# Kernel tuning notes

Measured on AMD Instinct MI355X. Metric: run time of the kernel, lower is better.

Reference implementation:

```python
import jax, jax.numpy as jnp
import numpy as np

H = W = 512
P = H * W          # total superpixel member pixels
N_SP = 1024        # number of superpixels


def _conv(x, w, b):
    # x: [N,C,H,W], w: [O,I,3,3] -> [N,O,H,W], SAME padding
    y = jax.lax.conv_general_dilated(
        x, w, window_strides=(1, 1), padding='SAME',
        dimension_numbers=('NCHW', 'OIHW', 'NCHW'))
    return y + b[None, :, None, None]


def _embed(raw, w1, b1, w2, b2, w3, b3):
    h = jax.nn.relu(_conv(raw, w1, b1))
    h = jax.nn.relu(_conv(h, w2, b2))
    return _conv(h, w3, b3)  # [1, 10, H, W]


def setup_inputs() -> dict:
    key = jax.random.key(0)
    ks = jax.random.split(key, 6)
    raw = jax.random.normal(ks[0], (1, 1, H, W), dtype=jnp.float32)
    w1 = jax.random.normal(ks[1], (64, 1, 3, 3), dtype=jnp.float32) * 0.3
    b1 = jnp.zeros((64,), jnp.float32)
    w2 = jax.random.normal(ks[2], (64, 64, 3, 3), dtype=jnp.float32) * 0.05
    b2 = jnp.zeros((64,), jnp.float32)
    w3 = jax.random.normal(ks[3], (10, 64, 3, 3), dtype=jnp.float32) * 0.05
    b3 = jnp.zeros((10,), jnp.float32)
    pix_rc = jax.random.randint(ks[4], (P, 2), 0, H, dtype=jnp.int32)
    seg_ids = jax.random.randint(ks[5], (P,), 0, N_SP, dtype=jnp.int32)
    return {"raw": raw, "w1": w1, "b1": b1, "w2": w2, "b2": b2,
            "w3": w3, "b3": b3, "pix_rc": pix_rc, "seg_ids": seg_ids,
            "n_sp": N_SP}


def reference(raw, w1, b1, w2, b2, w3, b3, pix_rc, seg_ids, n_sp):
    feats = _embed(raw, w1, b1, w2, b2, w3, b3)  # [1, C, H, W]
    f = feats[0]                                  # [C, H, W]
    # gather per-pixel feature vectors: [P, C]
    vals = f[:, pix_rc[:, 0], pix_rc[:, 1]].T
    # scatter-mean over superpixels (= per-sp sum / mass)
    sums = jax.ops.segment_sum(vals, seg_ids, num_segments=n_sp)      # [n_sp, C]
    cnts = jax.ops.segment_sum(jnp.ones((vals.shape[0],), vals.dtype),
                               seg_ids, num_segments=n_sp)            # [n_sp]
    return sums / jnp.maximum(cnts, 1.0)[:, None]
```

## Files before the change

kernel.cpp:

```cpp
#include <hip/hip_runtime.h>

typedef __attribute__((ext_vector_type(8))) short short8;
typedef __attribute__((ext_vector_type(4))) float f32x4;

constexpr int H = 512, W = 512;
constexpr int P = H * W;
constexpr int NSP = 1024;
constexpr int SBLK = 512;
constexpr int FGRP = 16;

__device__ inline unsigned short f2bf(float f) {
  unsigned u = __builtin_bit_cast(unsigned, f);
  unsigned r = (u + 0x7fffu + ((u >> 16) & 1u)) >> 16;
  return (unsigned short)r;
}
__device__ inline float bflo(unsigned u) { return __builtin_bit_cast(float, u << 16); }
__device__ inline float bfhi(unsigned u) { return __builtin_bit_cast(float, u & 0xffff0000u); }

__device__ inline int xcd_swz(int b, int cpx) { return (b & 7) * cpx + (b >> 3); }

__global__ __launch_bounds__(256) void prep_k(const float* __restrict__ w2,
                                              const float* __restrict__ w3,
                                              unsigned short* __restrict__ wt2s,
                                              unsigned short* __restrict__ wt3s) {
  int i = blockIdx.x * 256 + threadIdx.x;
  if (i < 36864) {
    int k = i >> 11;
    int t = (i >> 3) & 255;
    int e = i & 7;
    int r = t >> 2, sp = t & 3, s = sp ^ ((r >> 2) & 3);
    int tap = k >> 1, ic = (k & 1) * 32 + s * 8 + e;
    wt2s[i] = f2bf(w2[r * 576 + ic * 9 + tap]);
  } else if (i < 46080) {
    int j = i - 36864;
    int k = j >> 9;
    int t = (j >> 3) & 63;
    int e = j & 7;
    int r = t >> 2, sp = t & 3, s = sp ^ ((r >> 2) & 3);
    int tap = k >> 1, ic = (k & 1) * 32 + s * 8 + e;
    wt3s[j] = (r < 10) ? f2bf(w3[r * 576 + ic * 9 + tap]) : (unsigned short)0;
  }
}

__global__ __launch_bounds__(512, 4) void conv123_k(const float* __restrict__ raw,
                                                    const float* __restrict__ w1,
                                                    const float* __restrict__ b1,
                                                    const unsigned short* __restrict__ wts2,
                                                    const float* __restrict__ b2,
                                                    const unsigned short* __restrict__ wts3,
                                                    const float* __restrict__ b3,
                                                    unsigned short* __restrict__ feats) {
  constexpr int WCS = 2048;
  __shared__ __align__(16) unsigned short acts[448 * 64];
  __shared__ __align__(16) unsigned short wbuf[9216];
  __shared__ unsigned short rawtb[14 * 38 + 12];
  int tid = threadIdx.x;
  int lane = tid & 63, wave = tid >> 6;
  int logical = xcd_swz(blockIdx.x, 128);
  int tilex = logical & 15, tiley = logical >> 4;
  int c0 = tilex * 32, r0 = tiley * 8;

  if (tid < 256) {
#pragma unroll
    for (int k0 = 0; k0 < 3; ++k0) {
      const unsigned short* src = wts2 + (size_t)k0 * WCS + tid * 8;
      unsigned short* dstb = wbuf + (k0 & 3) * WCS + wave * 512;
      __builtin_amdgcn_global_load_lds((const __attribute__((address_space(1))) void*)src,
                                       (__attribute__((address_space(3))) void*)dstb, 16, 0, 0);
    }
  }
  for (int i = tid; i < 532; i += 512) {
    int rr = i / 38, cc = i - rr * 38;
    int gr = r0 + rr - 3, gc = c0 + cc - 3;
    bool ok = ((unsigned)gr < 512u) && ((unsigned)gc < 512u);
    rawtb[i] = ok ? f2bf(raw[gr * 512 + gc]) : (unsigned short)0;
  }

  int q = lane >> 4, n = lane & 15;
  int og1 = wave & 3;
  short8 a1f;
  {
    short av[8];
#pragma unroll
    for (int e = 0; e < 8; ++e) av[e] = 0;
    int oc = og1 * 16 + n;
    if (q == 0) {
#pragma unroll
      for (int e = 0; e < 8; ++e) av[e] = (short)f2bf(w1[oc * 9 + e]);
    } else if (q == 1) {
      av[0] = (short)f2bf(w1[oc * 9 + 8]);
    }
    a1f = (short8){av[0], av[1], av[2], av[3], av[4], av[5], av[6], av[7]};
  }
  float bb1[4];
#pragma unroll
  for (int r2 = 0; r2 < 4; ++r2) bb1[r2] = b1[og1 * 16 + q * 4 + r2];
  __syncthreads();

  char* actw = (char*)acts;
  int hhalf = wave >> 2;
  for (int i1 = 0; i1 < 14; ++i1) {
    int t = 2 * i1 + hhalf;
    if (t >= 27) break;
    int px = t * 16 + n;
    int py = px / 36, pxc = px - py * 36;
    short bv[8];
#pragma unroll
    for (int e = 0; e < 8; ++e) bv[e] = 0;
    if (q == 0) {
#pragma unroll
      for (int e = 0; e < 8; ++e) {
        int dy = e / 3, dx = e - dy * 3;
        bv[e] = (short)rawtb[(py + dy) * 38 + pxc + dx];
      }
    } else if (q == 1) {
      bv[0] = (short)rawtb[(py + 2) * 38 + pxc + 2];
    }
    short8 b1f = (short8){bv[0], bv[1], bv[2], bv[3], bv[4], bv[5], bv[6], bv[7]};
    f32x4 d = __builtin_amdgcn_mfma_f32_16x16x32_bf16(a1f, b1f,
                                                       (f32x4){0.f, 0.f, 0.f, 0.f}, 0, 0, 0);
    int gr1 = r0 + py - 2, gc1 = c0 + pxc - 2;
    bool ok1 = ((unsigned)gr1 < 512u) && ((unsigned)gc1 < 512u);
    float o0 = ok1 ? fmaxf(d.x + bb1[0], 0.f) : 0.f;
    float o1 = ok1 ? fmaxf(d.y + bb1[1], 0.f) : 0.f;
    float o2 = ok1 ? fmaxf(d.z + bb1[2], 0.f) : 0.f;
    float o3 = ok1 ? fmaxf(d.w + bb1[3], 0.f) : 0.f;
    unsigned lo = (unsigned)f2bf(o0) | ((unsigned)f2bf(o1) << 16);
    unsigned hi = (unsigned)f2bf(o2) | ((unsigned)f2bf(o3) << 16);
    int wa = px * 128 + ((((og1 * 2 + (q >> 1)) ^ (px & 7)) << 4)) + ((q & 1) << 3);
    *reinterpret_cast<uint2*>(actw + wa) = make_uint2(lo, hi);
  }
  __syncthreads();

  f32x4 acc[4][3];
#pragma unroll
  for (int og = 0; og < 4; ++og)
#pragma unroll
    for (int g = 0; g < 3; ++g) acc[og][g] = (f32x4){0.f, 0.f, 0.f, 0.f};
  const char* actb = (const char*)acts;

#pragma unroll
  for (int k = 0; k < 18; ++k) {
    if (k == 17) {
      asm volatile("s_waitcnt vmcnt(0)" ::: "memory");
    } else if (k == 16) {
      asm volatile("s_waitcnt vmcnt(1)" ::: "memory");
    } else {
      asm volatile("s_waitcnt vmcnt(2)" ::: "memory");
    }
    __builtin_amdgcn_sched_barrier(0);
    __builtin_amdgcn_s_barrier();
    __builtin_amdgcn_sched_barrier(0);
    if (k + 3 < 18 && tid < 256) {
      const unsigned short* src = wts2 + (size_t)(k + 3) * WCS + tid * 8;
      unsigned short* dstb = wbuf + ((k + 3) & 3) * WCS + wave * 512;
      __builtin_amdgcn_global_load_lds((const __attribute__((address_space(1))) void*)src,
                                       (__attribute__((address_space(3))) void*)dstb, 16, 0, 0);
    }
    const int tap = k >> 1, kc = k & 1;
    const int kyy = tap / 3, kxx = tap - kyy * 3;
    const char* wb = (const char*)(wbuf + (k & 3) * WCS);
    short8 af[4];
#pragma unroll
    for (int og = 0; og < 4; ++og) {
      int r = og * 16 + n;
      af[og] = *reinterpret_cast<const short8*>(wb + r * 64 + ((q ^ ((r >> 2) & 3)) * 16));
    }
#pragma unroll
    for (int g = 0; g < 3; ++g) {
      int t2 = wave + 8 * g;
      if (t2 < 23) {
        int pl = t2 * 16 + n + kyy * 36 + kxx;
        int addr = pl * 128 + (((kc * 4 + q) ^ (pl & 7)) * 16);
        short8 bf = *reinterpret_cast<const short8*>(actb + addr);
#pragma unroll
        for (int og = 0; og < 4; ++og)
          acc[og][g] = __builtin_amdgcn_mfma_f32_16x16x32_bf16(af[og], bf, acc[og][g], 0, 0, 0);
      }
    }
  }
  __syncthreads();

  for (int wi = wave; wi < 18; wi += 8) {
    const unsigned short* src = wts3 + (size_t)wi * 512 + lane * 8;
    unsigned short* dstb = &wbuf[wi * 512];
    __builtin_amdgcn_global_load_lds((const __attribute__((address_space(1))) void*)src,
                                     (__attribute__((address_space(3))) void*)dstb, 16, 0, 0);
  }
#pragma unroll
  for (int g = 0; g < 3; ++g) {
    int t2 = wave + 8 * g;
    if (t2 < 23) {
      int px2 = t2 * 16 + n;
#pragma unroll
      for (int og = 0; og < 4; ++og) {
        f32x4 v = acc[og][g];
        float o0 = fmaxf(v.x + b2[og * 16 + q * 4 + 0], 0.f);
        float o1 = fmaxf(v.y + b2[og * 16 + q * 4 + 1], 0.f);
        float o2 = fmaxf(v.z + b2[og * 16 + q * 4 + 2], 0.f);
        float o3 = fmaxf(v.w + b2[og * 16 + q * 4 + 3], 0.f);
        unsigned lo = (unsigned)f2bf(o0) | ((unsigned)f2bf(o1) << 16);
        unsigned hi = (unsigned)f2bf(o2) | ((unsigned)f2bf(o3) << 16);
        int lslot = og * 2 + (q >> 1);
        int wa = px2 * 128 + (((lslot ^ (px2 & 7)) << 4)) + ((q & 1) << 3);
        *reinterpret_cast<uint2*>(actw + wa) = make_uint2(lo, hi);
      }
    }
  }
  __syncthreads();

  f32x4 acc3[2];
#pragma unroll
  for (int g = 0; g < 2; ++g) acc3[g] = (f32x4){0.f, 0.f, 0.f, 0.f};
  const char* wb3 = (const char*)wbuf;

#pragma unroll
  for (int k = 0; k < 18; ++k) {
    const int tap = k >> 1, kc = k & 1;
    const int kyy = tap / 3, kxx = tap - kyy * 3;
    short8 af = *reinterpret_cast<const short8*>(wb3 + k * 1024 + n * 64 +
                                                 ((q ^ ((n >> 2) & 3)) * 16));
#pragma unroll
    for (int g = 0; g < 2; ++g) {
      int pl = wave * 36 + g * 16 + n + kyy * 36 + kxx;
      int addr = pl * 128 + (((kc * 4 + q) ^ (pl & 7)) * 16);
      short8 bf = *reinterpret_cast<const short8*>(actb + addr);
      acc3[g] = __builtin_amdgcn_mfma_f32_16x16x32_bf16(af, bf, acc3[g], 0, 0, 0);
    }
  }

  __syncthreads();
  char* ob = (char*)acts;
  float bb3[4];
#pragma unroll
  for (int r2 = 0; r2 < 4; ++r2) {
    int oc = q * 4 + r2;
    bb3[r2] = (oc < 10) ? b3[oc] : 0.f;
  }
#pragma unroll
  for (int g = 0; g < 2; ++g) {
    int pl = wave * 32 + g * 16 + n;
    f32x4 v = acc3[g];
    float o0 = v.x + bb3[0], o1 = v.y + bb3[1], o2 = v.z + bb3[2], o3 = v.w + bb3[3];
    if (q < 2) {
      unsigned u0 = (unsigned)f2bf(o0) | ((unsigned)f2bf(o1) << 16);
      unsigned u1 = (unsigned)f2bf(o2) | ((unsigned)f2bf(o3) << 16);
      *reinterpret_cast<uint2*>(ob + pl * 24 + q * 8) = make_uint2(u0, u1);
    } else if (q == 2) {
      *reinterpret_cast<unsigned*>(ob + pl * 24 + 16) =
          (unsigned)f2bf(o0) | ((unsigned)f2bf(o1) << 16);
    }
  }
  __syncthreads();
  char* fb = (char*)feats;
#pragma unroll
  for (int it = 0; it < 3; ++it) {
    int c = it * 512 + tid;
    if (c < 1280) {
      int row = c / 160, wb = c - row * 160;
      int byte = wb * 4;
      int px = byte / 20, off = byte - px * 20;
      unsigned v = *reinterpret_cast<const unsigned*>(ob + (row * 32 + px) * 24 + off);
      size_t gbyte = (((size_t)(r0 + row) * 512) + c0) * 20 + (size_t)byte;
      *reinterpret_cast<unsigned*>(fb + gbyte) = v;
    }
  }
}

__global__ __launch_bounds__(512) void scatter_k(const unsigned short* __restrict__ feats,
                                                 const int* __restrict__ pix_rc,
                                                 const int* __restrict__ seg,
                                                 float* __restrict__ partials) {
  __shared__ float ls[NSP * 10];
  __shared__ float lc[NSP];
  int tid = threadIdx.x;
  for (int i = tid; i < NSP * 10; i += 512) ls[i] = 0.f;
  for (int i = tid; i < NSP; i += 512) lc[i] = 0.f;
  __syncthreads();

  constexpr int PER = P / SBLK;
  int p0 = blockIdx.x * PER;
  for (int p = p0 + tid; p < p0 + PER; p += 512) {
    int r = pix_rc[2 * p], c = pix_rc[2 * p + 1];
    int s = seg[p];
    size_t gpix = (size_t)r * 512 + c;
    const char* fp = (const char*)feats + gpix * 20;
    uint4 a = *reinterpret_cast<const uint4*>(fp);
    unsigned e = *reinterpret_cast<const unsigned*>(fp + 16);
    float v[10];
    v[0] = bflo(a.x); v[1] = bfhi(a.x);
    v[2] = bflo(a.y); v[3] = bfhi(a.y);
    v[4] = bflo(a.z); v[5] = bfhi(a.z);
    v[6] = bflo(a.w); v[7] = bfhi(a.w);
    v[8] = bflo(e);   v[9] = bfhi(e);
#pragma unroll
    for (int ch = 0; ch < 10; ++ch) atomicAdd(&ls[s * 10 + ch], v[ch]);
    atomicAdd(&lc[s], 1.f);
  }
  __syncthreads();

  float* outp = partials + (size_t)blockIdx.x * (NSP * 11);
  for (int i = tid; i < NSP * 10; i += 512) outp[i] = ls[i];
  for (int i = tid; i < NSP; i += 512) outp[NSP * 10 + i] = lc[i];
}

__global__ __launch_bounds__(256) void finA_k(const float* __restrict__ partials,
                                              float* __restrict__ partials2) {
  int g = blockIdx.x / 44;
  int e = (blockIdx.x - g * 44) * 256 + threadIdx.x;
  const float* base = partials + (size_t)(g * 32) * (NSP * 11) + e;
  float s = 0.f;
#pragma unroll 8
  for (int k = 0; k < 32; ++k) s += base[(size_t)k * (NSP * 11)];
  partials2[(size_t)g * (NSP * 11) + e] = s;
}

__global__ __launch_bounds__(256) void finB_k(const float* __restrict__ partials2,
                                              float* __restrict__ out) {
  int i = blockIdx.x * 256 + threadIdx.x;
  if (i >= NSP * 10) return;
  int sp = i / 10;
  float s = 0.f, cnt = 0.f;
#pragma unroll
  for (int g = 0; g < FGRP; ++g) {
    const float* pp = partials2 + (size_t)g * (NSP * 11);
    s += pp[i];
    cnt += pp[NSP * 10 + sp];
  }
  out[i] = s / fmaxf(cnt, 1.f);
}

extern "C" void kernel_launch(void* const* d_in, const int* in_sizes, int n_in,
                              void* d_out, int out_size, void* d_ws, size_t ws_size,
                              hipStream_t stream) {
  const float* raw = (const float*)d_in[0];
  const float* w1  = (const float*)d_in[1];
  const float* b1  = (const float*)d_in[2];
  const float* w2  = (const float*)d_in[3];
  const float* b2  = (const float*)d_in[4];
  const float* w3  = (const float*)d_in[5];
  const float* b3  = (const float*)d_in[6];
  const int* pix_rc = (const int*)d_in[7];
  const int* seg    = (const int*)d_in[8];
  float* out = (float*)d_out;

  char* ws = (char*)d_ws;
  float* partials  = (float*)(ws + 0);
  float* partials2 = (float*)(ws + 23068672);
  unsigned short* feats = (unsigned short*)(ws + 25165824);
  unsigned short* wt2s = (unsigned short*)(ws + 30408704);
  unsigned short* wt3s = (unsigned short*)(ws + 30482432);

  prep_k<<<180, 256, 0, stream>>>(w2, w3, wt2s, wt3s);
  conv123_k<<<1024, 512, 0, stream>>>(raw, w1, b1, wt2s, b2, wt3s, b3, feats);
  scatter_k<<<SBLK, 512, 0, stream>>>(feats, pix_rc, seg, partials);
  finA_k<<<FGRP * 44, 256, 0, stream>>>(partials, partials2);
  finB_k<<<40, 256, 0, stream>>>(partials2, out);
}
```

Measured before the change: 83.27 us.

## Halve scatter blocks, fuse two-stage reduction, add MFMA priority hints

Scatter now runs on 256 blocks instead of 512, which halves the per-block partial buffers that have to be reduced. The two finalize kernels become one kernel in which each block reduces 128 partials per half and combines the halves through shared memory. The conv kernel wraps its MFMA loops in s_setprio so waves issuing matrix ops get scheduling priority. The pixel coordinate load is vectorised to int2. Fewer scatter blocks mean less parallelism and more LDS atomic contention per block, and the single finalize kernel launches only 80 blocks, each doing longer serial loads.

```diff
diff --git a/kernel.cpp b/kernel.cpp
--- a/kernel.cpp
+++ b/kernel.cpp
@@ -6,8 +6,8 @@
 constexpr int H = 512, W = 512;
 constexpr int P = H * W;
 constexpr int NSP = 1024;
-constexpr int SBLK = 512;
-constexpr int FGRP = 16;
+constexpr int SBLK = 256;
+constexpr int PROW = NSP * 11;
 
 __device__ inline unsigned short f2bf(float f) {
   unsigned u = __builtin_bit_cast(unsigned, f);
@@ -166,6 +166,7 @@
       int r = og * 16 + n;
       af[og] = *reinterpret_cast<const short8*>(wb + r * 64 + ((q ^ ((r >> 2) & 3)) * 16));
     }
+    __builtin_amdgcn_s_setprio(1);
 #pragma unroll
     for (int g = 0; g < 3; ++g) {
       int t2 = wave + 8 * g;
@@ -178,6 +179,7 @@
           acc[og][g] = __builtin_amdgcn_mfma_f32_16x16x32_bf16(af[og], bf, acc[og][g], 0, 0, 0);
       }
     }
+    __builtin_amdgcn_s_setprio(0);
   }
   __syncthreads();
 
@@ -214,6 +216,7 @@
   for (int g = 0; g < 2; ++g) acc3[g] = (f32x4){0.f, 0.f, 0.f, 0.f};
   const char* wb3 = (const char*)wbuf;
 
+  __builtin_amdgcn_s_setprio(1);
 #pragma unroll
   for (int k = 0; k < 18; ++k) {
     const int tap = k >> 1, kc = k & 1;
@@ -228,6 +231,7 @@
       acc3[g] = __builtin_amdgcn_mfma_f32_16x16x32_bf16(af, bf, acc3[g], 0, 0, 0);
     }
   }
+  __builtin_amdgcn_s_setprio(0);
 
   __syncthreads();
   char* ob = (char*)acts;
@@ -281,9 +285,9 @@
   constexpr int PER = P / SBLK;
   int p0 = blockIdx.x * PER;
   for (int p = p0 + tid; p < p0 + PER; p += 512) {
-    int r = pix_rc[2 * p], c = pix_rc[2 * p + 1];
+    int2 rc = *reinterpret_cast<const int2*>(pix_rc + 2 * p);
     int s = seg[p];
-    size_t gpix = (size_t)r * 512 + c;
+    size_t gpix = (size_t)rc.x * 512 + rc.y;
     const char* fp = (const char*)feats + gpix * 20;
     uint4 a = *reinterpret_cast<const uint4*>(fp);
     unsigned e = *reinterpret_cast<const unsigned*>(fp + 16);
@@ -299,35 +303,34 @@
   }
   __syncthreads();
 
-  float* outp = partials + (size_t)blockIdx.x * (NSP * 11);
+  float* outp = partials + (size_t)blockIdx.x * PROW;
   for (int i = tid; i < NSP * 10; i += 512) outp[i] = ls[i];
   for (int i = tid; i < NSP; i += 512) outp[NSP * 10 + i] = lc[i];
 }
 
-__global__ __launch_bounds__(256) void finA_k(const float* __restrict__ partials,
-                                              float* __restrict__ partials2) {
-  int g = blockIdx.x / 44;
-  int e = (blockIdx.x - g * 44) * 256 + threadIdx.x;
-  const float* base = partials + (size_t)(g * 32) * (NSP * 11) + e;
-  float s = 0.f;
+__global__ __launch_bounds__(256) void fin_k(const float* __restrict__ partials,
+                                             float* __restrict__ out) {
+  __shared__ float red[2][128][2];
+  int t = threadIdx.x;
+  int oi = t & 127, h = t >> 7;
+  int o = blockIdx.x * 128 + oi;
+  int sp = o / 10;
+  const float* base = partials + (size_t)h * 128 * PROW;
+  float s = 0.f, cnt = 0.f;
 #pragma unroll 8
-  for (int k = 0; k < 32; ++k) s += base[(size_t)k * (NSP * 11)];
-  partials2[(size_t)g * (NSP * 11) + e] = s;
-}
-
-__global__ __launch_bounds__(256) void finB_k(const float* __restrict__ partials2,
-                                              float* __restrict__ out) {
-  int i = blockIdx.x * 256 + threadIdx.x;
-  if (i >= NSP * 10) return;
-  int sp = i / 10;
-  float s = 0.f, cnt = 0.f;
-#pragma unroll
-  for (int g = 0; g < FGRP; ++g) {
-    const float* pp = partials2 + (size_t)g * (NSP * 11);
-    s += pp[i];
+  for (int k = 0; k < 128; ++k) {
+    const float* pp = base + (size_t)k * PROW;
+    s += pp[o];
     cnt += pp[NSP * 10 + sp];
   }
-  out[i] = s / fmaxf(cnt, 1.f);
+  red[h][oi][0] = s;
+  red[h][oi][1] = cnt;
+  __syncthreads();
+  if (h == 0) {
+    float st = red[0][oi][0] + red[1][oi][0];
+    float ct = red[0][oi][1] + red[1][oi][1];
+    out[o] = st / fmaxf(ct, 1.f);
+  }
 }
 
 extern "C" void kernel_launch(void* const* d_in, const int* in_sizes, int n_in,
@@ -346,7 +349,6 @@
 
   char* ws = (char*)d_ws;
   float* partials  = (float*)(ws + 0);
-  float* partials2 = (float*)(ws + 23068672);
   unsigned short* feats = (unsigned short*)(ws + 25165824);
   unsigned short* wt2s = (unsigned short*)(ws + 30408704);
   unsigned short* wt3s = (unsigned short*)(ws + 30482432);
@@ -354,6 +356,5 @@
   prep_k<<<180, 256, 0, stream>>>(w2, w3, wt2s, wt3s);
   conv123_k<<<1024, 512, 0, stream>>>(raw, w1, b1, wt2s, b2, wt3s, b3, feats);
   scatter_k<<<SBLK, 512, 0, stream>>>(feats, pix_rc, seg, partials);
-  finA_k<<<FGRP * 44, 256, 0, stream>>>(partials, partials2);
-  finB_k<<<40, 256, 0, stream>>>(partials2, out);
-}
+  fin_k<<<80, 256, 0, stream>>>(partials, out);
+}
```

New measurement: 89.76 us. +7.8%, slower.
